# Kernel tuning notes

Measured on AMD Instinct MI355X. Metric: run time of the kernel, lower is better.

The kernel has to match this reference:

```python
import jax, jax.numpy as jnp
import numpy as np

B, HW, ENC = 64, 14, 2048
T_CAP, VOCAB = 25, 10000
EMB = DEC = ATT = 512


def setup_inputs() -> dict:
    key = jax.random.key(0)
    ks = jax.random.split(key, 24)
    n = lambda k, shape, s=0.02: jax.random.normal(k, shape, jnp.float32) * s
    encoder_out = jax.random.normal(ks[0], (B, HW, HW, ENC), jnp.float32)
    captions = jax.random.randint(ks[1], (B, T_CAP), 0, VOCAB)
    lens = jax.random.randint(ks[2], (B,), 2, T_CAP + 1)
    caption_lengths = jnp.sort(lens)[::-1].at[0].set(T_CAP)  # sorted desc, max=T_CAP
    return {
        'encoder_out': encoder_out,
        'captions': captions,
        'caption_lengths': caption_lengths,
        'emb': jax.random.uniform(ks[3], (VOCAB, EMB), jnp.float32, -0.1, 0.1),
        'We_att': n(ks[4], (ENC, ATT)), 'be_att': jnp.zeros((ATT,), jnp.float32),
        'Wd_att': n(ks[5], (DEC, ATT)), 'bd_att': jnp.zeros((ATT,), jnp.float32),
        'v_att': n(ks[6], (ATT, 1)),    'bv_att': jnp.zeros((1,), jnp.float32),
        'W_ih': n(ks[7], (4 * DEC, EMB + ENC)), 'b_ih': jnp.zeros((4 * DEC,), jnp.float32),
        'W_hh': n(ks[8], (4 * DEC, DEC)),       'b_hh': jnp.zeros((4 * DEC,), jnp.float32),
        'W_init_h': n(ks[9], (ENC, DEC)),  'b_init_h': jnp.zeros((DEC,), jnp.float32),
        'W_init_c': n(ks[10], (ENC, DEC)), 'b_init_c': jnp.zeros((DEC,), jnp.float32),
        'W_fbeta': n(ks[11], (DEC, ENC)),  'b_fbeta': jnp.zeros((ENC,), jnp.float32),
        'W_fc': jax.random.uniform(ks[12], (DEC, VOCAB), jnp.float32, -0.1, 0.1),
        'b_fc': jnp.zeros((VOCAB,), jnp.float32),
    }


def reference(encoder_out, captions, caption_lengths, emb,
              We_att, be_att, Wd_att, bd_att, v_att, bv_att,
              W_ih, b_ih, W_hh, b_hh,
              W_init_h, b_init_h, W_init_c, b_init_c,
              W_fbeta, b_fbeta, W_fc, b_fc):
    Bn = encoder_out.shape[0]
    enc = encoder_out.reshape(Bn, -1, encoder_out.shape[-1])  # [B, P=196, ENC]
    decode_lengths = caption_lengths - 1
    T = captions.shape[1] - 1  # static max(decode_lengths)

    emb_cap = emb[captions]                    # [B, T+1, EMB]
    mean_enc = enc.mean(axis=1)                # [B, ENC]
    h0 = mean_enc @ W_init_h + b_init_h        # [B, DEC]
    c0 = mean_enc @ W_init_c + b_init_c
    att1 = enc @ We_att + be_att               # [B, P, ATT], hoisted (same math each step)

    def step(carry, inp):
        h, c = carry
        x_emb, active = inp                    # [B,EMB], [B] bool (batch_size_t mask)
        # attention
        att2 = h @ Wd_att + bd_att             # [B, ATT]
        e = (jax.nn.relu(att1 + att2[:, None, :]) @ v_att)[..., 0] + bv_att[0]  # [B, P]
        alpha = jax.nn.softmax(e, axis=1)
        ctx = jnp.einsum('bp,bpe->be', alpha, enc)
        # gated context
        ctx = jax.nn.sigmoid(h @ W_fbeta + b_fbeta) * ctx
        # LSTMCell (torch gate order i, f, g, o)
        x = jnp.concatenate([x_emb, ctx], axis=1)
        g = x @ W_ih.T + b_ih + h @ W_hh.T + b_hh
        i_g, f_g, g_g, o_g = jnp.split(g, 4, axis=1)
        c_new = jax.nn.sigmoid(f_g) * c + jax.nn.sigmoid(i_g) * jnp.tanh(g_g)
        h_new = jax.nn.sigmoid(o_g) * jnp.tanh(c_new)
        pred = h_new @ W_fc + b_fc             # dropout = identity (eval)
        m = active[:, None]
        pred = jnp.where(m, pred, 0.0)         # padded rows stay zero (as in torch)
        alpha = jnp.where(m, alpha, 0.0)
        h = jnp.where(m, h_new, h)
        c = jnp.where(m, c_new, c)
        return (h, c), (pred, alpha)

    active_ts = jnp.arange(T)[:, None] < decode_lengths[None, :]   # [T, B]
    xs = (jnp.swapaxes(emb_cap[:, :T], 0, 1), active_ts)
    _, (preds, alphas) = jax.lax.scan(step, (h0, c0), xs)
    predictions = jnp.swapaxes(preds, 0, 1)    # [B, T, VOCAB]
    alphas = jnp.swapaxes(alphas, 0, 1)        # [B, T, P]
    return predictions, captions, decode_lengths, alphas
```

## Files before the change

### kernel.cpp

```cpp
#include <hip/hip_runtime.h>
#include <hip/hip_bf16.h>

#define BATCH 64
#define NPIX 196
#define ENCD 2048
#define ATTD 512
#define DECD 512
#define EMBD 512
#define NVOCAB 10000
#define TSTEPS 24
#define KX 3072
#define NPAD 10112

typedef short bf16x8 __attribute__((ext_vector_type(8)));
typedef float f32x4 __attribute__((ext_vector_type(4)));

__device__ inline ushort f2bf(float f) {
    union { float f; unsigned u; } v; v.f = f;
    unsigned r = (v.u + 0x7fff + ((v.u >> 16) & 1)) >> 16;
    return (ushort)r;
}
__device__ inline float bf2f(ushort u) {
    union { unsigned u; float f; } v; v.u = ((unsigned)u) << 16;
    return v.f;
}

__global__ __launch_bounds__(256) void k_prep(
        const float* __restrict__ Wih, const float* __restrict__ Whh,
        const float* __restrict__ Wd, const float* __restrict__ Wfb,
        const float* __restrict__ Wfc, const float* __restrict__ We,
        const float* __restrict__ emb, const int* __restrict__ caps,
        const int* __restrict__ lens,
        ushort* __restrict__ WTj, ushort* __restrict__ BpreT,
        ushort* __restrict__ WfcT, ushort* __restrict__ WeT,
        ushort* __restrict__ embpartb, float* __restrict__ hcacc,
        float* __restrict__ cap_out, float* __restrict__ len_out) {
    __shared__ float tile[64][65];
    int blk = blockIdx.x, tid = threadIdx.x;
    int tx = tid & 63, ty = tid >> 6;
    int fx = tid & 15, fy = tid >> 4;
    if (blk < 2048) {
        int j = blk;
        for (int k = 512 + tid; k < KX; k += 256) {
            float v = (k < 2560) ? Wih[(size_t)j * 2560 + k] : Whh[(size_t)j * 512 + (k - 2560)];
            WTj[(size_t)j * KX + k] = f2bf(v);
        }
        if (blk == 0) {
            for (int i = tid; i < 1664; i += 256) {
                if (i < 1600) cap_out[i] = (float)caps[i];
                else          len_out[i - 1600] = (float)(lens[i - 1600] - 1);
            }
        }
    } else if (blk < 2368) {
        int i = blk - 2048;
        int nb = (i % 40) * 64, kb = (i / 40) * 64;
        for (int s = 0; s < 4; ++s) {
            int k = kb + fy + s * 16;
            int n = nb + fx * 4;
            float4 v = (n < ATTD) ? *(const float4*)(Wd + (size_t)k * ATTD + n)
                                  : *(const float4*)(Wfb + (size_t)k * ENCD + (n - ATTD));
            tile[fy + s * 16][fx * 4 + 0] = v.x;
            tile[fy + s * 16][fx * 4 + 1] = v.y;
            tile[fy + s * 16][fx * 4 + 2] = v.z;
            tile[fy + s * 16][fx * 4 + 3] = v.w;
        }
        __syncthreads();
        for (int s = 0; s < 64; s += 4)
            BpreT[(size_t)(nb + ty + s) * 512 + kb + tx] = f2bf(tile[tx][ty + s]);
    } else if (blk < 3632) {
        int i = blk - 2368;
        int nb = (i % 158) * 64, kb = (i / 158) * 64;
        for (int s = 0; s < 4; ++s) {
            int k = kb + fy + s * 16;
            int n = nb + fx * 4;
            float4 v = make_float4(0.f, 0.f, 0.f, 0.f);
            if (n < NVOCAB) v = *(const float4*)(Wfc + (size_t)k * NVOCAB + n);
            tile[fy + s * 16][fx * 4 + 0] = v.x;
            tile[fy + s * 16][fx * 4 + 1] = v.y;
            tile[fy + s * 16][fx * 4 + 2] = v.z;
            tile[fy + s * 16][fx * 4 + 3] = v.w;
        }
        __syncthreads();
        for (int s = 0; s < 64; s += 4)
            WfcT[(size_t)(nb + ty + s) * 512 + kb + tx] = f2bf(tile[tx][ty + s]);
    } else if (blk < 3888) {
        int i = blk - 3632;
        int nb = (i % 8) * 64, kb = (i / 8) * 64;
        for (int s = 0; s < 4; ++s) {
            int k = kb + fy + s * 16;
            int n = nb + fx * 4;
            float4 v = *(const float4*)(We + (size_t)k * ATTD + n);
            tile[fy + s * 16][fx * 4 + 0] = v.x;
            tile[fy + s * 16][fx * 4 + 1] = v.y;
            tile[fy + s * 16][fx * 4 + 2] = v.z;
            tile[fy + s * 16][fx * 4 + 3] = v.w;
        }
        __syncthreads();
        for (int s = 0; s < 64; s += 4)
            WeT[(size_t)(nb + ty + s) * ENCD + kb + tx] = f2bf(tile[tx][ty + s]);
    } else if (blk < 4656) {
        int i = blk - 3888;
        int r0 = (i % 24) * 64;
        int n0 = (i / 24) * 64;
        int w = tid >> 6, l = tid & 63;
        int m = l & 15, kg = l >> 4;
        int n = n0 + w * 16 + m;
        const float* Bp = Wih + (size_t)n * 2560 + kg * 8;
        int tok[4];
#pragma unroll
        for (int mf = 0; mf < 4; ++mf) {
            int row = r0 + m + mf * 16;
            tok[mf] = caps[(row & 63) * 25 + (row >> 6)];
        }
        f32x4 acc[4] = {};
        for (int k0 = 0; k0 < 512; k0 += 32) {
            float4 b0 = *(const float4*)(Bp + k0);
            float4 b1 = *(const float4*)(Bp + k0 + 4);
            bf16x8 bb;
            bb[0] = f2bf(b0.x); bb[1] = f2bf(b0.y); bb[2] = f2bf(b0.z); bb[3] = f2bf(b0.w);
            bb[4] = f2bf(b1.x); bb[5] = f2bf(b1.y); bb[6] = f2bf(b1.z); bb[7] = f2bf(b1.w);
#pragma unroll
            for (int mf = 0; mf < 4; ++mf) {
                const float* ap = emb + (size_t)tok[mf] * 512 + kg * 8 + k0;
                float4 f0 = *(const float4*)ap;
                float4 f1 = *(const float4*)(ap + 4);
                bf16x8 a;
                a[0] = f2bf(f0.x); a[1] = f2bf(f0.y); a[2] = f2bf(f0.z); a[3] = f2bf(f0.w);
                a[4] = f2bf(f1.x); a[5] = f2bf(f1.y); a[6] = f2bf(f1.z); a[7] = f2bf(f1.w);
                acc[mf] = __builtin_amdgcn_mfma_f32_16x16x32_bf16(a, bb, acc[mf], 0, 0, 0);
            }
        }
#pragma unroll
        for (int mf = 0; mf < 4; ++mf)
#pragma unroll
            for (int r = 0; r < 4; ++r)
                embpartb[(size_t)(r0 + mf * 16 + kg * 4 + r) * 2048 + n] = f2bf(acc[mf][r]);
    } else {
        int i = blk - 4656;
        for (int j = tid; j < 2048; j += 256) hcacc[(size_t)i * 2048 + j] = 0.f;
    }
}

__global__ void k_encconv(const float* __restrict__ enc, ushort* __restrict__ encb) {
    size_t i = ((size_t)blockIdx.x * 256 + threadIdx.x) * 8;
    float4 f0 = *(const float4*)(enc + i);
    float4 f1 = *(const float4*)(enc + i + 4);
    union { bf16x8 v; ushort u[8]; } o;
    o.u[0] = f2bf(f0.x); o.u[1] = f2bf(f0.y); o.u[2] = f2bf(f0.z); o.u[3] = f2bf(f0.w);
    o.u[4] = f2bf(f1.x); o.u[5] = f2bf(f1.y); o.u[6] = f2bf(f1.z); o.u[7] = f2bf(f1.w);
    *(bf16x8*)(encb + i) = o.v;
}

__global__ __launch_bounds__(256) void k_meanb(const ushort* __restrict__ encb,
                                               ushort* __restrict__ meanb) {
    int b = blockIdx.x, half = blockIdx.y;
    int e0 = half * 1024 + threadIdx.x * 4;
    const ushort* ep = encb + (size_t)b * NPIX * ENCD + e0;
    float s0 = 0.f, s1 = 0.f, s2 = 0.f, s3 = 0.f;
#pragma unroll 4
    for (int p = 0; p < NPIX; ++p) {
        ushort4 v = *(const ushort4*)(ep + (size_t)p * ENCD);
        s0 += bf2f(v.x); s1 += bf2f(v.y); s2 += bf2f(v.z); s3 += bf2f(v.w);
    }
    const float sc = 1.0f / NPIX;
    ushort4 o;
    o.x = f2bf(s0 * sc); o.y = f2bf(s1 * sc); o.z = f2bf(s2 * sc); o.w = f2bf(s3 * sc);
    *(ushort4*)(meanb + (size_t)b * ENCD + e0) = o;
}

__global__ __launch_bounds__(256) void k_initp(
        const ushort* __restrict__ meanb,
        const float* __restrict__ Wh, const float* __restrict__ Wc,
        float* __restrict__ hcacc) {
    __shared__ float mm[4][256];
    int bg = blockIdx.x * 4;
    int jy = blockIdx.y;
    int kz = blockIdx.z;
    int tid = threadIdx.x;
    for (int i = tid; i < 1024; i += 256) {
        int qq = i >> 8, k = i & 255;
        mm[qq][k] = bf2f(meanb[(size_t)(bg + qq) * ENCD + kz * 256 + k]);
    }
    __syncthreads();
    int j = jy * 256 + tid;
    const float* W; int col;
    if (j < 512) { W = Wh; col = j; } else { W = Wc; col = j - 512; }
    W += (size_t)(kz * 256) * 512 + col;
    float acc[4] = {};
    for (int k = 0; k < 256; ++k) {
        float w = W[(size_t)k * 512];
#pragma unroll
        for (int qq = 0; qq < 4; ++qq) acc[qq] += mm[qq][k] * w;
    }
#pragma unroll
    for (int qq = 0; qq < 4; ++qq)
        atomicAdd(hcacc + (size_t)(bg + qq) * 1024 + j, acc[qq]);
}

__global__ __launch_bounds__(256) void k_initfin(
        const float* __restrict__ hcacc, const float* __restrict__ bh,
        const float* __restrict__ bc, ushort* __restrict__ hbf,
        float* __restrict__ c) {
    int base = blockIdx.x * 2048;
    for (int i = threadIdx.x; i < 2048; i += 256) {
        int idx = base + i;
        int b = idx >> 10, n = idx & 1023;
        float v = hcacc[idx];
        if (n < 512) hbf[(size_t)b * 512 + n] = f2bf(v + bh[n]);
        else         c[(size_t)b * 512 + (n - 512)] = v + bc[n - 512];
    }
}

__global__ __launch_bounds__(512) void k_att1(
        const ushort* __restrict__ encb, const ushort* __restrict__ WeT,
        const float* __restrict__ be, ushort* __restrict__ att1b) {
    __shared__ float red[4][64][65];
    int bid = blockIdx.x;
    int L = (bid & 7) * 49 + (bid >> 3);
    int mt = L >> 2, nt = L & 3;
    int tid = threadIdx.x;
    int w = tid >> 6, l = tid & 63;
    int q = w & 3, kh = w >> 2;
    int wr = q >> 1, wc = q & 1;
    int m0 = mt * 128 + wr * 64;
    int n0 = nt * 128 + wc * 64;
    int ml = l & 15, kg = l >> 4;
    const ushort* aBase = encb + (size_t)(m0 + ml) * ENCD + kh * 1024 + kg * 8;
    const ushort* bBase = WeT + (size_t)(n0 + ml) * ENCD + kh * 1024 + kg * 8;
    f32x4 acc[4][4] = {};
    for (int k0 = 0; k0 < 1024; k0 += 32) {
        bf16x8 bfr[4], afr[4];
#pragma unroll
        for (int nf = 0; nf < 4; ++nf)
            bfr[nf] = *(const bf16x8*)(bBase + (size_t)nf * 16 * ENCD + k0);
#pragma unroll
        for (int mf = 0; mf < 4; ++mf)
            afr[mf] = *(const bf16x8*)(aBase + (size_t)mf * 16 * ENCD + k0);
#pragma unroll
        for (int mf = 0; mf < 4; ++mf)
#pragma unroll
            for (int nf = 0; nf < 4; ++nf)
                acc[mf][nf] = __builtin_amdgcn_mfma_f32_16x16x32_bf16(afr[mf], bfr[nf], acc[mf][nf], 0, 0, 0);
    }
    if (kh == 1) {
#pragma unroll
        for (int mf = 0; mf < 4; ++mf)
#pragma unroll
            for (int nf = 0; nf < 4; ++nf)
#pragma unroll
                for (int r = 0; r < 4; ++r)
                    red[q][mf * 16 + kg * 4 + r][nf * 16 + ml] = acc[mf][nf][r];
    }
    __syncthreads();
    if (kh == 0) {
#pragma unroll
        for (int mf = 0; mf < 4; ++mf)
#pragma unroll
            for (int nf = 0; nf < 4; ++nf) {
                int col = n0 + nf * 16 + ml;
                float bias = be[col];
#pragma unroll
                for (int r = 0; r < 4; ++r) {
                    int row = m0 + mf * 16 + kg * 4 + r;
                    float v = acc[mf][nf][r] + red[q][mf * 16 + kg * 4 + r][nf * 16 + ml];
                    att1b[(size_t)row * ATTD + col] = f2bf(v + bias);
                }
            }
    }
}

__global__ __launch_bounds__(512) void k_hsmall2(
        const ushort* __restrict__ hb_cur, const ushort* __restrict__ BpreT,
        const float* __restrict__ bd, const float* __restrict__ bfb,
        float* __restrict__ att2, ushort* __restrict__ gateb) {
    __shared__ float part[2][64][68];
    int blk = blockIdx.x;
    int tid = threadIdx.x;
    int w = tid >> 6, l = tid & 63;
    int wq = w & 3, kh = w >> 2;
    int m = l & 15, kg = l >> 4;
    int n = blk * 64 + wq * 16 + m;
    const ushort* B = BpreT + (size_t)n * 512 + kh * 256 + kg * 8;
    const ushort* A = hb_cur + (size_t)m * 512 + kh * 256 + kg * 8;
    f32x4 acc[4] = {};
#pragma unroll
    for (int k0 = 0; k0 < 256; k0 += 32) {
        bf16x8 bfr = *(const bf16x8*)(B + k0);
#pragma unroll
        for (int mf = 0; mf < 4; ++mf) {
            bf16x8 afr = *(const bf16x8*)(A + mf * 16 * 512 + k0);
            acc[mf] = __builtin_amdgcn_mfma_f32_16x16x32_bf16(afr, bfr, acc[mf], 0, 0, 0);
        }
    }
#pragma unroll
    for (int mf = 0; mf < 4; ++mf)
#pragma unroll
        for (int r = 0; r < 4; ++r)
            part[kh][mf * 16 + kg * 4 + r][wq * 16 + m] = acc[mf][r];
    __syncthreads();
    for (int idx = tid; idx < 4096; idx += 512) {
        int b = idx >> 6, nn = idx & 63;
        float v = part[0][b][nn] + part[1][b][nn];
        int ng = blk * 64 + nn;
        if (ng < 512) att2[(size_t)b * 512 + ng] = v + bd[ng];
        else {
            int e = ng - 512;
            gateb[(size_t)b * 2048 + e] = f2bf(1.f / (1.f + __expf(-(v + bfb[e]))));
        }
    }
}

__global__ __launch_bounds__(512) void k_scorectx(
        const ushort* __restrict__ att1b, const float* __restrict__ att2,
        const float* __restrict__ vatt, const float* __restrict__ bv,
        const ushort* __restrict__ gateb, const int* __restrict__ lens,
        const ushort* __restrict__ encb,
        ushort* __restrict__ ctxb, float* __restrict__ alpha_out, int t) {
    __shared__ float ev[200];
    __shared__ float cpart[4][512];
    __shared__ float inv_s;
    int bid = blockIdx.x;
    int b = ((bid & 7) << 3) | ((bid >> 3) & 7);
    int q = bid >> 6;
    int tid = threadIdx.x;
    int w = tid >> 6, l = tid & 63;
    if (t >= lens[b] - 1) {
        if (q == 0 && tid < NPIX)
            alpha_out[((size_t)b * TSTEPS + t) * NPIX + tid] = 0.f;
        return;
    }
    {
        float a2r[8], vvr[8];
        const float* att2b = att2 + (size_t)b * ATTD;
#pragma unroll
        for (int i = 0; i < 8; ++i) {
            a2r[i] = att2b[l * 8 + i];
            vvr[i] = vatt[l * 8 + i];
        }
        float bv0 = bv[0];
        for (int pp = w; pp < NPIX; pp += 8) {
            bf16x8 f = *(const bf16x8*)(att1b + ((size_t)b * NPIX + pp) * ATTD + l * 8);
            float s = 0.f;
#pragma unroll
            for (int i = 0; i < 8; ++i)
                s += fmaxf(bf2f((ushort)f[i]) + a2r[i], 0.f) * vvr[i];
            for (int off = 32; off > 0; off >>= 1) s += __shfl_down(s, off);
            if (l == 0) ev[pp] = s + bv0;
        }
    }
    __syncthreads();
    if (w == 0) {
        float mx = -1e30f;
        for (int pp = l; pp < NPIX; pp += 64) mx = fmaxf(mx, ev[pp]);
        for (int off = 32; off > 0; off >>= 1) mx = fmaxf(mx, __shfl_down(mx, off));
        mx = __shfl(mx, 0);
        float s = 0.f;
        for (int pp = l; pp < NPIX; pp += 64) {
            float e_ = __expf(ev[pp] - mx);
            ev[pp] = e_;
            s += e_;
        }
        for (int off = 32; off > 0; off >>= 1) s += __shfl_down(s, off);
        if (l == 0) inv_s = 1.0f / s;
    }
    __syncthreads();
    float inv = inv_s;
    if (q == 0 && tid < NPIX)
        alpha_out[((size_t)b * TSTEPS + t) * NPIX + tid] = ev[tid] * inv;
    {
        int pg = tid >> 7, th = tid & 127;
        const ushort* ep = encb + (size_t)b * NPIX * ENCD + q * 512 + th * 4;
        float s0 = 0.f, s1 = 0.f, s2 = 0.f, s3 = 0.f;
        for (int pp = pg; pp < NPIX; pp += 4) {
            ushort4 v = *(const ushort4*)(ep + (size_t)pp * ENCD);
            float al = ev[pp];
            s0 += al * bf2f(v.x); s1 += al * bf2f(v.y);
            s2 += al * bf2f(v.z); s3 += al * bf2f(v.w);
        }
        cpart[pg][th * 4 + 0] = s0;
        cpart[pg][th * 4 + 1] = s1;
        cpart[pg][th * 4 + 2] = s2;
        cpart[pg][th * 4 + 3] = s3;
    }
    __syncthreads();
    if (tid < 128) {
        ushort4 g4 = *(const ushort4*)(gateb + (size_t)b * 2048 + q * 512 + tid * 4);
        ushort4 o;
        o.x = f2bf((cpart[0][tid * 4 + 0] + cpart[1][tid * 4 + 0] + cpart[2][tid * 4 + 0] + cpart[3][tid * 4 + 0]) * inv * bf2f(g4.x));
        o.y = f2bf((cpart[0][tid * 4 + 1] + cpart[1][tid * 4 + 1] + cpart[2][tid * 4 + 1] + cpart[3][tid * 4 + 1]) * inv * bf2f(g4.y));
        o.z = f2bf((cpart[0][tid * 4 + 2] + cpart[1][tid * 4 + 2] + cpart[2][tid * 4 + 2] + cpart[3][tid * 4 + 2]) * inv * bf2f(g4.z));
        o.w = f2bf((cpart[0][tid * 4 + 3] + cpart[1][tid * 4 + 3] + cpart[2][tid * 4 + 3] + cpart[3][tid * 4 + 3]) * inv * bf2f(g4.w));
        *(ushort4*)(ctxb + (size_t)b * 2048 + q * 512 + tid * 4) = o;
    }
}

__global__ __launch_bounds__(512) void k_gates2(
        const ushort* __restrict__ ctxb, const ushort* __restrict__ hb_cur,
        const ushort* __restrict__ WTj, const ushort* __restrict__ embpartb,
        const float* __restrict__ bih, const float* __restrict__ bhh,
        const int* __restrict__ lens, float* __restrict__ c,
        ushort* __restrict__ hb_nxt, ushort* __restrict__ hAll, int t) {
    __shared__ float part[8][64][16];
    int g = blockIdx.x;
    int tid = threadIdx.x;
    int w = tid >> 6, l = tid & 63;
    int m = l & 15, kg = l >> 4;
    int jrow = (m >> 2) * 512 + g * 4 + (m & 3);
    const ushort* Brow = WTj + (size_t)jrow * KX;
    f32x4 acc[4] = {};
    {
        const ushort* B = Brow + 512 + w * 256 + kg * 8;
        const ushort* A = ctxb + (size_t)m * 2048 + w * 256 + kg * 8;
#pragma unroll
        for (int k0 = 0; k0 < 256; k0 += 32) {
            bf16x8 bfr = *(const bf16x8*)(B + k0);
#pragma unroll
            for (int mf = 0; mf < 4; ++mf) {
                bf16x8 afr = *(const bf16x8*)(A + (size_t)mf * 16 * 2048 + k0);
                acc[mf] = __builtin_amdgcn_mfma_f32_16x16x32_bf16(afr, bfr, acc[mf], 0, 0, 0);
            }
        }
    }
    {
        const ushort* B = Brow + 2560 + w * 64 + kg * 8;
        const ushort* A = hb_cur + (size_t)m * 512 + w * 64 + kg * 8;
#pragma unroll
        for (int k0 = 0; k0 < 64; k0 += 32) {
            bf16x8 bfr = *(const bf16x8*)(B + k0);
#pragma unroll
            for (int mf = 0; mf < 4; ++mf) {
                bf16x8 afr = *(const bf16x8*)(A + (size_t)mf * 16 * 512 + k0);
                acc[mf] = __builtin_amdgcn_mfma_f32_16x16x32_bf16(afr, bfr, acc[mf], 0, 0, 0);
            }
        }
    }
#pragma unroll
    for (int mf = 0; mf < 4; ++mf)
#pragma unroll
        for (int r = 0; r < 4; ++r)
            part[w][mf * 16 + kg * 4 + r][m] = acc[mf][r];
    __syncthreads();
    if (tid < 256) {
        int bb = tid >> 2, j = tid & 3;
        int d = g * 4 + j;
        float gi = 0.f, gf = 0.f, gg = 0.f, go = 0.f;
#pragma unroll
        for (int w8 = 0; w8 < 8; ++w8) {
            gi += part[w8][bb][j];
            gf += part[w8][bb][4 + j];
            gg += part[w8][bb][8 + j];
            go += part[w8][bb][12 + j];
        }
        ushort hout = hb_cur[(size_t)bb * 512 + d];
        if (t < lens[bb] - 1) {
            const ushort* eb = embpartb + ((size_t)t * 64 + bb) * 2048;
            gi += bf2f(eb[d])        + bih[d]        + bhh[d];
            gf += bf2f(eb[512 + d])  + bih[512 + d]  + bhh[512 + d];
            gg += bf2f(eb[1024 + d]) + bih[1024 + d] + bhh[1024 + d];
            go += bf2f(eb[1536 + d]) + bih[1536 + d] + bhh[1536 + d];
            float cc = c[(size_t)bb * 512 + d];
            float si = 1.f / (1.f + __expf(-gi));
            float sf = 1.f / (1.f + __expf(-gf));
            float so = 1.f / (1.f + __expf(-go));
            float cn = sf * cc + si * tanhf(gg);
            float hn = so * tanhf(cn);
            c[(size_t)bb * 512 + d] = cn;
            hout = f2bf(hn);
        }
        hb_nxt[(size_t)bb * 512 + d] = hout;
        hAll[((size_t)t * 64 + bb) * 512 + d] = hout;
    }
}

__global__ __launch_bounds__(256) void k_predall(
        const ushort* __restrict__ hAll, const ushort* __restrict__ WfcT,
        const float* __restrict__ bfc, const int* __restrict__ lens,
        float* __restrict__ pred) {
    int w = threadIdx.x >> 6, l = threadIdx.x & 63;
    int wr = w >> 1, wc = w & 1;
    int m0 = blockIdx.x * 128 + wr * 64;
    int n0 = blockIdx.y * 128 + wc * 64;
    int ml = l & 15, kg = l >> 4;
    const ushort* aBase = hAll + (size_t)(m0 + ml) * 512 + kg * 8;
    const ushort* bBase = WfcT + (size_t)(n0 + ml) * 512 + kg * 8;
    f32x4 acc[4][4] = {};
#pragma unroll 2
    for (int k0 = 0; k0 < 512; k0 += 32) {
        bf16x8 bfr[4], afr[4];
#pragma unroll
        for (int nf = 0; nf < 4; ++nf)
            bfr[nf] = *(const bf16x8*)(bBase + (size_t)nf * 16 * 512 + k0);
#pragma unroll
        for (int mf = 0; mf < 4; ++mf)
            afr[mf] = *(const bf16x8*)(aBase + (size_t)mf * 16 * 512 + k0);
#pragma unroll
        for (int mf = 0; mf < 4; ++mf)
#pragma unroll
            for (int nf = 0; nf < 4; ++nf)
                acc[mf][nf] = __builtin_amdgcn_mfma_f32_16x16x32_bf16(afr[mf], bfr[nf], acc[mf][nf], 0, 0, 0);
    }
#pragma unroll
    for (int mf = 0; mf < 4; ++mf)
#pragma unroll
        for (int nf = 0; nf < 4; ++nf) {
            int col = n0 + nf * 16 + ml;
            if (col < NVOCAB) {
                float bias = bfc[col];
#pragma unroll
                for (int r = 0; r < 4; ++r) {
                    int row = m0 + mf * 16 + kg * 4 + r;
                    int t = row >> 6, b = row & 63;
                    bool act = t < (lens[b] - 1);
                    pred[((size_t)b * TSTEPS + t) * NVOCAB + col] = act ? acc[mf][nf][r] + bias : 0.f;
                }
            }
        }
}

extern "C" void kernel_launch(void* const* d_in, const int* in_sizes, int n_in,
                              void* d_out, int out_size, void* d_ws, size_t ws_size,
                              hipStream_t stream) {
    const float* enc  = (const float*)d_in[0];
    const int*   caps = (const int*)d_in[1];
    const int*   lens = (const int*)d_in[2];
    const float* emb  = (const float*)d_in[3];
    const float* We   = (const float*)d_in[4];
    const float* be   = (const float*)d_in[5];
    const float* Wd   = (const float*)d_in[6];
    const float* bd   = (const float*)d_in[7];
    const float* vatt = (const float*)d_in[8];
    const float* bv   = (const float*)d_in[9];
    const float* Wih  = (const float*)d_in[10];
    const float* bih  = (const float*)d_in[11];
    const float* Whh  = (const float*)d_in[12];
    const float* bhh  = (const float*)d_in[13];
    const float* Winh = (const float*)d_in[14];
    const float* binh = (const float*)d_in[15];
    const float* Winc = (const float*)d_in[16];
    const float* binc = (const float*)d_in[17];
    const float* Wfb  = (const float*)d_in[18];
    const float* bfb  = (const float*)d_in[19];
    const float* Wfc  = (const float*)d_in[20];
    const float* bfc  = (const float*)d_in[21];

    float* out       = (float*)d_out;
    float* pred_out  = out;
    float* cap_out   = out + 15360000;
    float* len_out   = out + 15361600;
    float* alpha_out = out + 15361664;

    char* p = (char*)d_ws;
    ushort* att1b    = (ushort*)p; p += (size_t)12544 * 512 * 2;
    ushort* WTj      = (ushort*)p; p += (size_t)2048 * KX * 2;
    ushort* WfcT     = (ushort*)p; p += (size_t)NPAD * 512 * 2;
    ushort* BpreT    = (ushort*)p; p += (size_t)2560 * 512 * 2;
    ushort* WeT      = (ushort*)p; p += (size_t)512 * 2048 * 2;
    ushort* embpartb = (ushort*)p; p += (size_t)1536 * 2048 * 2;
    ushort* hAll     = (ushort*)p; p += (size_t)1536 * 512 * 2;
    ushort* ctxb     = (ushort*)p; p += (size_t)64 * 2048 * 2;
    ushort* hb0      = (ushort*)p; p += (size_t)64 * 512 * 2;
    ushort* hb1      = (ushort*)p; p += (size_t)64 * 512 * 2;
    float* c         = (float*)p;  p += (size_t)64 * 512 * 4;
    ushort* meanb    = (ushort*)p; p += (size_t)64 * 2048 * 2;
    float* att2      = (float*)p;  p += (size_t)64 * 512 * 4;
    ushort* gateb    = (ushort*)p; p += (size_t)64 * 2048 * 2;
    ushort* encb     = (ushort*)p; p += (size_t)64 * NPIX * ENCD * 2;
    float* hcacc     = (float*)ctxb;

    k_prep<<<4688, 256, 0, stream>>>(Wih, Whh, Wd, Wfb, Wfc, We, emb, caps, lens,
                                     WTj, BpreT, WfcT, WeT, embpartb, hcacc,
                                     cap_out, len_out);
    k_encconv<<<12544, 256, 0, stream>>>(enc, encb);
    k_meanb<<<dim3(64, 2), 256, 0, stream>>>(encb, meanb);
    k_initp<<<dim3(16, 4, 8), 256, 0, stream>>>(meanb, Winh, Winc, hcacc);
    k_initfin<<<32, 256, 0, stream>>>(hcacc, binh, binc, hb0, c);
    k_att1<<<392, 512, 0, stream>>>(encb, WeT, be, att1b);

    for (int t = 0; t < TSTEPS; ++t) {
        const ushort* hcur = (t & 1) ? hb1 : hb0;
        ushort* hnxt = (t & 1) ? hb0 : hb1;
        k_hsmall2<<<40, 512, 0, stream>>>(hcur, BpreT, bd, bfb, att2, gateb);
        k_scorectx<<<256, 512, 0, stream>>>(att1b, att2, vatt, bv, gateb, lens,
                                            encb, ctxb, alpha_out, t);
        k_gates2<<<128, 512, 0, stream>>>(ctxb, hcur, WTj, embpartb, bih, bhh,
                                          lens, c, hnxt, hAll, t);
    }
    k_predall<<<dim3(12, 79), 256, 0, stream>>>(hAll, WfcT, bfc, lens, pred_out);
}
```

Baseline: 1.778 ms.

## Fuse per-step attention and LSTM kernels into one launch with flag-based inter-block sync

```diff
diff --git a/kernel.cpp b/kernel.cpp
--- a/kernel.cpp
+++ b/kernel.cpp
@@ -34,6 +34,7 @@
         ushort* __restrict__ WTj, ushort* __restrict__ BpreT,
         ushort* __restrict__ WfcT, ushort* __restrict__ WeT,
         ushort* __restrict__ embpartb, float* __restrict__ hcacc,
+        int* __restrict__ flags,
         float* __restrict__ cap_out, float* __restrict__ len_out) {
     __shared__ float tile[64][65];
     int blk = blockIdx.x, tid = threadIdx.x;
@@ -138,6 +139,7 @@
     } else {
         int i = blk - 4656;
         for (int j = tid; j < 2048; j += 256) hcacc[(size_t)i * 2048 + j] = 0.f;
+        if (i == 0 && tid < 64) flags[tid] = 0;
     }
 }
 
@@ -211,24 +213,21 @@
     }
 }
 
-__global__ __launch_bounds__(512) void k_att1(
+__global__ __launch_bounds__(256) void k_att1(
         const ushort* __restrict__ encb, const ushort* __restrict__ WeT,
         const float* __restrict__ be, ushort* __restrict__ att1b) {
-    __shared__ float red[4][64][65];
     int bid = blockIdx.x;
     int L = (bid & 7) * 49 + (bid >> 3);
     int mt = L >> 2, nt = L & 3;
-    int tid = threadIdx.x;
-    int w = tid >> 6, l = tid & 63;
-    int q = w & 3, kh = w >> 2;
-    int wr = q >> 1, wc = q & 1;
+    int w = threadIdx.x >> 6, l = threadIdx.x & 63;
+    int wr = w >> 1, wc = w & 1;
     int m0 = mt * 128 + wr * 64;
     int n0 = nt * 128 + wc * 64;
     int ml = l & 15, kg = l >> 4;
-    const ushort* aBase = encb + (size_t)(m0 + ml) * ENCD + kh * 1024 + kg * 8;
-    const ushort* bBase = WeT + (size_t)(n0 + ml) * ENCD + kh * 1024 + kg * 8;
+    const ushort* aBase = encb + (size_t)(m0 + ml) * ENCD + kg * 8;
+    const ushort* bBase = WeT + (size_t)(n0 + ml) * ENCD + kg * 8;
     f32x4 acc[4][4] = {};
-    for (int k0 = 0; k0 < 1024; k0 += 32) {
+    for (int k0 = 0; k0 < ENCD; k0 += 32) {
         bf16x8 bfr[4], afr[4];
 #pragma unroll
         for (int nf = 0; nf < 4; ++nf)
@@ -242,233 +241,242 @@
             for (int nf = 0; nf < 4; ++nf)
                 acc[mf][nf] = __builtin_amdgcn_mfma_f32_16x16x32_bf16(afr[mf], bfr[nf], acc[mf][nf], 0, 0, 0);
     }
-    if (kh == 1) {
-#pragma unroll
-        for (int mf = 0; mf < 4; ++mf)
-#pragma unroll
-            for (int nf = 0; nf < 4; ++nf)
-#pragma unroll
-                for (int r = 0; r < 4; ++r)
-                    red[q][mf * 16 + kg * 4 + r][nf * 16 + ml] = acc[mf][nf][r];
-    }
-    __syncthreads();
-    if (kh == 0) {
-#pragma unroll
-        for (int mf = 0; mf < 4; ++mf)
-#pragma unroll
-            for (int nf = 0; nf < 4; ++nf) {
-                int col = n0 + nf * 16 + ml;
-                float bias = be[col];
-#pragma unroll
-                for (int r = 0; r < 4; ++r) {
-                    int row = m0 + mf * 16 + kg * 4 + r;
-                    float v = acc[mf][nf][r] + red[q][mf * 16 + kg * 4 + r][nf * 16 + ml];
-                    att1b[(size_t)row * ATTD + col] = f2bf(v + bias);
-                }
-            }
-    }
-}
-
-__global__ __launch_bounds__(512) void k_hsmall2(
-        const ushort* __restrict__ hb_cur, const ushort* __restrict__ BpreT,
+#pragma unroll
+    for (int mf = 0; mf < 4; ++mf)
+#pragma unroll
+        for (int nf = 0; nf < 4; ++nf) {
+            int col = n0 + nf * 16 + ml;
+            float bias = be[col];
+#pragma unroll
+            for (int r = 0; r < 4; ++r) {
+                int row = m0 + mf * 16 + kg * 4 + r;
+                att1b[(size_t)row * ATTD + col] = f2bf(acc[mf][nf][r] + bias);
+            }
+        }
+}
+
+__global__ __launch_bounds__(512) void k_step(
+        const ushort* __restrict__ att1b, const ushort* __restrict__ encb,
+        const ushort* __restrict__ BpreT, const ushort* __restrict__ WTj,
+        const ushort* __restrict__ embpartb,
+        const float* __restrict__ vatt, const float* __restrict__ bv,
         const float* __restrict__ bd, const float* __restrict__ bfb,
-        float* __restrict__ att2, ushort* __restrict__ gateb) {
-    __shared__ float part[2][64][68];
-    int blk = blockIdx.x;
-    int tid = threadIdx.x;
-    int w = tid >> 6, l = tid & 63;
-    int wq = w & 3, kh = w >> 2;
-    int m = l & 15, kg = l >> 4;
-    int n = blk * 64 + wq * 16 + m;
-    const ushort* B = BpreT + (size_t)n * 512 + kh * 256 + kg * 8;
-    const ushort* A = hb_cur + (size_t)m * 512 + kh * 256 + kg * 8;
-    f32x4 acc[4] = {};
-#pragma unroll
-    for (int k0 = 0; k0 < 256; k0 += 32) {
-        bf16x8 bfr = *(const bf16x8*)(B + k0);
-#pragma unroll
-        for (int mf = 0; mf < 4; ++mf) {
-            bf16x8 afr = *(const bf16x8*)(A + mf * 16 * 512 + k0);
-            acc[mf] = __builtin_amdgcn_mfma_f32_16x16x32_bf16(afr, bfr, acc[mf], 0, 0, 0);
-        }
-    }
-#pragma unroll
-    for (int mf = 0; mf < 4; ++mf)
-#pragma unroll
-        for (int r = 0; r < 4; ++r)
-            part[kh][mf * 16 + kg * 4 + r][wq * 16 + m] = acc[mf][r];
-    __syncthreads();
-    for (int idx = tid; idx < 4096; idx += 512) {
-        int b = idx >> 6, nn = idx & 63;
-        float v = part[0][b][nn] + part[1][b][nn];
-        int ng = blk * 64 + nn;
-        if (ng < 512) att2[(size_t)b * 512 + ng] = v + bd[ng];
-        else {
-            int e = ng - 512;
-            gateb[(size_t)b * 2048 + e] = f2bf(1.f / (1.f + __expf(-(v + bfb[e]))));
-        }
-    }
-}
-
-__global__ __launch_bounds__(512) void k_scorectx(
-        const ushort* __restrict__ att1b, const float* __restrict__ att2,
-        const float* __restrict__ vatt, const float* __restrict__ bv,
-        const ushort* __restrict__ gateb, const int* __restrict__ lens,
-        const ushort* __restrict__ encb,
-        ushort* __restrict__ ctxb, float* __restrict__ alpha_out, int t) {
-    __shared__ float ev[200];
-    __shared__ float cpart[4][512];
-    __shared__ float inv_s;
+        const float* __restrict__ bih, const float* __restrict__ bhh,
+        const int* __restrict__ lens,
+        const ushort* __restrict__ hb_cur, ushort* __restrict__ hb_nxt,
+        float* __restrict__ c, ushort* __restrict__ hAll,
+        float* __restrict__ att2, ushort* __restrict__ gateb,
+        ushort* __restrict__ ctxb, float* __restrict__ alpha_out,
+        int* __restrict__ flags, int t) {
+    __shared__ char smem_raw[34816];
     int bid = blockIdx.x;
-    int b = ((bid & 7) << 3) | ((bid >> 3) & 7);
-    int q = bid >> 6;
-    int tid = threadIdx.x;
-    int w = tid >> 6, l = tid & 63;
-    if (t >= lens[b] - 1) {
-        if (q == 0 && tid < NPIX)
-            alpha_out[((size_t)b * TSTEPS + t) * NPIX + tid] = 0.f;
-        return;
-    }
-    {
-        float a2r[8], vvr[8];
-        const float* att2b = att2 + (size_t)b * ATTD;
-#pragma unroll
-        for (int i = 0; i < 8; ++i) {
-            a2r[i] = att2b[l * 8 + i];
-            vvr[i] = vatt[l * 8 + i];
-        }
-        float bv0 = bv[0];
-        for (int pp = w; pp < NPIX; pp += 8) {
-            bf16x8 f = *(const bf16x8*)(att1b + ((size_t)b * NPIX + pp) * ATTD + l * 8);
-            float s = 0.f;
-#pragma unroll
-            for (int i = 0; i < 8; ++i)
-                s += fmaxf(bf2f((ushort)f[i]) + a2r[i], 0.f) * vvr[i];
-            for (int off = 32; off > 0; off >>= 1) s += __shfl_down(s, off);
-            if (l == 0) ev[pp] = s + bv0;
-        }
-    }
-    __syncthreads();
-    if (w == 0) {
-        float mx = -1e30f;
-        for (int pp = l; pp < NPIX; pp += 64) mx = fmaxf(mx, ev[pp]);
-        for (int off = 32; off > 0; off >>= 1) mx = fmaxf(mx, __shfl_down(mx, off));
-        mx = __shfl(mx, 0);
-        float s = 0.f;
-        for (int pp = l; pp < NPIX; pp += 64) {
-            float e_ = __expf(ev[pp] - mx);
-            ev[pp] = e_;
-            s += e_;
-        }
-        for (int off = 32; off > 0; off >>= 1) s += __shfl_down(s, off);
-        if (l == 0) inv_s = 1.0f / s;
-    }
-    __syncthreads();
-    float inv = inv_s;
-    if (q == 0 && tid < NPIX)
-        alpha_out[((size_t)b * TSTEPS + t) * NPIX + tid] = ev[tid] * inv;
-    {
-        int pg = tid >> 7, th = tid & 127;
-        const ushort* ep = encb + (size_t)b * NPIX * ENCD + q * 512 + th * 4;
-        float s0 = 0.f, s1 = 0.f, s2 = 0.f, s3 = 0.f;
-        for (int pp = pg; pp < NPIX; pp += 4) {
-            ushort4 v = *(const ushort4*)(ep + (size_t)pp * ENCD);
-            float al = ev[pp];
-            s0 += al * bf2f(v.x); s1 += al * bf2f(v.y);
-            s2 += al * bf2f(v.z); s3 += al * bf2f(v.w);
-        }
-        cpart[pg][th * 4 + 0] = s0;
-        cpart[pg][th * 4 + 1] = s1;
-        cpart[pg][th * 4 + 2] = s2;
-        cpart[pg][th * 4 + 3] = s3;
-    }
-    __syncthreads();
-    if (tid < 128) {
-        ushort4 g4 = *(const ushort4*)(gateb + (size_t)b * 2048 + q * 512 + tid * 4);
-        ushort4 o;
-        o.x = f2bf((cpart[0][tid * 4 + 0] + cpart[1][tid * 4 + 0] + cpart[2][tid * 4 + 0] + cpart[3][tid * 4 + 0]) * inv * bf2f(g4.x));
-        o.y = f2bf((cpart[0][tid * 4 + 1] + cpart[1][tid * 4 + 1] + cpart[2][tid * 4 + 1] + cpart[3][tid * 4 + 1]) * inv * bf2f(g4.y));
-        o.z = f2bf((cpart[0][tid * 4 + 2] + cpart[1][tid * 4 + 2] + cpart[2][tid * 4 + 2] + cpart[3][tid * 4 + 2]) * inv * bf2f(g4.z));
-        o.w = f2bf((cpart[0][tid * 4 + 3] + cpart[1][tid * 4 + 3] + cpart[2][tid * 4 + 3] + cpart[3][tid * 4 + 3]) * inv * bf2f(g4.w));
-        *(ushort4*)(ctxb + (size_t)b * 2048 + q * 512 + tid * 4) = o;
-    }
-}
-
-__global__ __launch_bounds__(512) void k_gates2(
-        const ushort* __restrict__ ctxb, const ushort* __restrict__ hb_cur,
-        const ushort* __restrict__ WTj, const ushort* __restrict__ embpartb,
-        const float* __restrict__ bih, const float* __restrict__ bhh,
-        const int* __restrict__ lens, float* __restrict__ c,
-        ushort* __restrict__ hb_nxt, ushort* __restrict__ hAll, int t) {
-    __shared__ float part[8][64][16];
-    int g = blockIdx.x;
     int tid = threadIdx.x;
     int w = tid >> 6, l = tid & 63;
     int m = l & 15, kg = l >> 4;
-    int jrow = (m >> 2) * 512 + g * 4 + (m & 3);
-    const ushort* Brow = WTj + (size_t)jrow * KX;
-    f32x4 acc[4] = {};
-    {
-        const ushort* B = Brow + 512 + w * 256 + kg * 8;
-        const ushort* A = ctxb + (size_t)m * 2048 + w * 256 + kg * 8;
+    int* flag0 = flags + 2 * t;
+    int* flag1 = flags + 2 * t + 1;
+
+    if (bid < 40) {
+        float (*part)[64][68] = (float (*)[64][68])smem_raw;
+        int blk = bid;
+        int wq = w & 3, kh = w >> 2;
+        int n = blk * 64 + wq * 16 + m;
+        const ushort* B = BpreT + (size_t)n * 512 + kh * 256 + kg * 8;
+        const ushort* A = hb_cur + (size_t)m * 512 + kh * 256 + kg * 8;
+        f32x4 acc[4] = {};
 #pragma unroll
         for (int k0 = 0; k0 < 256; k0 += 32) {
             bf16x8 bfr = *(const bf16x8*)(B + k0);
 #pragma unroll
             for (int mf = 0; mf < 4; ++mf) {
-                bf16x8 afr = *(const bf16x8*)(A + (size_t)mf * 16 * 2048 + k0);
+                bf16x8 afr = *(const bf16x8*)(A + mf * 16 * 512 + k0);
                 acc[mf] = __builtin_amdgcn_mfma_f32_16x16x32_bf16(afr, bfr, acc[mf], 0, 0, 0);
             }
         }
-    }
-    {
-        const ushort* B = Brow + 2560 + w * 64 + kg * 8;
-        const ushort* A = hb_cur + (size_t)m * 512 + w * 64 + kg * 8;
-#pragma unroll
-        for (int k0 = 0; k0 < 64; k0 += 32) {
-            bf16x8 bfr = *(const bf16x8*)(B + k0);
-#pragma unroll
-            for (int mf = 0; mf < 4; ++mf) {
-                bf16x8 afr = *(const bf16x8*)(A + (size_t)mf * 16 * 512 + k0);
-                acc[mf] = __builtin_amdgcn_mfma_f32_16x16x32_bf16(afr, bfr, acc[mf], 0, 0, 0);
-            }
-        }
-    }
-#pragma unroll
-    for (int mf = 0; mf < 4; ++mf)
-#pragma unroll
-        for (int r = 0; r < 4; ++r)
-            part[w][mf * 16 + kg * 4 + r][m] = acc[mf][r];
-    __syncthreads();
-    if (tid < 256) {
-        int bb = tid >> 2, j = tid & 3;
-        int d = g * 4 + j;
-        float gi = 0.f, gf = 0.f, gg = 0.f, go = 0.f;
-#pragma unroll
-        for (int w8 = 0; w8 < 8; ++w8) {
-            gi += part[w8][bb][j];
-            gf += part[w8][bb][4 + j];
-            gg += part[w8][bb][8 + j];
-            go += part[w8][bb][12 + j];
-        }
-        ushort hout = hb_cur[(size_t)bb * 512 + d];
-        if (t < lens[bb] - 1) {
-            const ushort* eb = embpartb + ((size_t)t * 64 + bb) * 2048;
-            gi += bf2f(eb[d])        + bih[d]        + bhh[d];
-            gf += bf2f(eb[512 + d])  + bih[512 + d]  + bhh[512 + d];
-            gg += bf2f(eb[1024 + d]) + bih[1024 + d] + bhh[1024 + d];
-            go += bf2f(eb[1536 + d]) + bih[1536 + d] + bhh[1536 + d];
-            float cc = c[(size_t)bb * 512 + d];
-            float si = 1.f / (1.f + __expf(-gi));
-            float sf = 1.f / (1.f + __expf(-gf));
-            float so = 1.f / (1.f + __expf(-go));
-            float cn = sf * cc + si * tanhf(gg);
-            float hn = so * tanhf(cn);
-            c[(size_t)bb * 512 + d] = cn;
-            hout = f2bf(hn);
-        }
-        hb_nxt[(size_t)bb * 512 + d] = hout;
-        hAll[((size_t)t * 64 + bb) * 512 + d] = hout;
+#pragma unroll
+        for (int mf = 0; mf < 4; ++mf)
+#pragma unroll
+            for (int r = 0; r < 4; ++r)
+                part[kh][mf * 16 + kg * 4 + r][wq * 16 + m] = acc[mf][r];
+        __syncthreads();
+        for (int idx = tid; idx < 4096; idx += 512) {
+            int b = idx >> 6, nn = idx & 63;
+            float v = part[0][b][nn] + part[1][b][nn];
+            int ng = blk * 64 + nn;
+            if (ng < 512) att2[(size_t)b * 512 + ng] = v + bd[ng];
+            else {
+                int e = ng - 512;
+                gateb[(size_t)b * 2048 + e] = f2bf(1.f / (1.f + __expf(-(v + bfb[e]))));
+            }
+        }
+        __syncthreads();
+        if (tid == 0) {
+            __threadfence();
+            __hip_atomic_fetch_add(flag0, 1, __ATOMIC_RELEASE, __HIP_MEMORY_SCOPE_AGENT);
+        }
+    } else if (bid < 296) {
+        float* ev = (float*)smem_raw;
+        float* cpart = ev + 200;
+        float* inv_sp = cpart + 2048;
+        int bid2 = bid - 40;
+        int b = ((bid2 & 7) << 3) | ((bid2 >> 3) & 7);
+        int q = bid2 >> 6;
+        if (t >= lens[b] - 1) {
+            if (q == 0 && tid < NPIX)
+                alpha_out[((size_t)b * TSTEPS + t) * NPIX + tid] = 0.f;
+            __syncthreads();
+            if (tid == 0) {
+                __threadfence();
+                __hip_atomic_fetch_add(flag1, 1, __ATOMIC_RELEASE, __HIP_MEMORY_SCOPE_AGENT);
+            }
+            return;
+        }
+        float vvr[8];
+#pragma unroll
+        for (int i = 0; i < 8; ++i) vvr[i] = vatt[l * 8 + i];
+        float bv0 = bv[0];
+        if (tid == 0) {
+            while (__hip_atomic_load(flag0, __ATOMIC_ACQUIRE, __HIP_MEMORY_SCOPE_AGENT) < 40)
+                __builtin_amdgcn_s_sleep(8);
+        }
+        __syncthreads();
+        {
+            float a2r[8];
+            const float* att2b = att2 + (size_t)b * ATTD;
+#pragma unroll
+            for (int i = 0; i < 8; ++i) a2r[i] = att2b[l * 8 + i];
+            for (int pp = w; pp < NPIX; pp += 8) {
+                bf16x8 f = *(const bf16x8*)(att1b + ((size_t)b * NPIX + pp) * ATTD + l * 8);
+                float s = 0.f;
+#pragma unroll
+                for (int i = 0; i < 8; ++i)
+                    s += fmaxf(bf2f((ushort)f[i]) + a2r[i], 0.f) * vvr[i];
+                for (int off = 32; off > 0; off >>= 1) s += __shfl_down(s, off);
+                if (l == 0) ev[pp] = s + bv0;
+            }
+        }
+        __syncthreads();
+        if (w == 0) {
+            float mx = -1e30f;
+            for (int pp = l; pp < NPIX; pp += 64) mx = fmaxf(mx, ev[pp]);
+            for (int off = 32; off > 0; off >>= 1) mx = fmaxf(mx, __shfl_down(mx, off));
+            mx = __shfl(mx, 0);
+            float s = 0.f;
+            for (int pp = l; pp < NPIX; pp += 64) {
+                float e_ = __expf(ev[pp] - mx);
+                ev[pp] = e_;
+                s += e_;
+            }
+            for (int off = 32; off > 0; off >>= 1) s += __shfl_down(s, off);
+            if (l == 0) *inv_sp = 1.0f / s;
+        }
+        __syncthreads();
+        float inv = *inv_sp;
+        if (q == 0 && tid < NPIX)
+            alpha_out[((size_t)b * TSTEPS + t) * NPIX + tid] = ev[tid] * inv;
+        {
+            int pg = tid >> 7, th = tid & 127;
+            const ushort* ep = encb + (size_t)b * NPIX * ENCD + q * 512 + th * 4;
+            float s0 = 0.f, s1 = 0.f, s2 = 0.f, s3 = 0.f;
+            for (int pp = pg; pp < NPIX; pp += 4) {
+                ushort4 v = *(const ushort4*)(ep + (size_t)pp * ENCD);
+                float al = ev[pp];
+                s0 += al * bf2f(v.x); s1 += al * bf2f(v.y);
+                s2 += al * bf2f(v.z); s3 += al * bf2f(v.w);
+            }
+            cpart[pg * 512 + th * 4 + 0] = s0;
+            cpart[pg * 512 + th * 4 + 1] = s1;
+            cpart[pg * 512 + th * 4 + 2] = s2;
+            cpart[pg * 512 + th * 4 + 3] = s3;
+        }
+        __syncthreads();
+        if (tid < 128) {
+            ushort4 g4 = *(const ushort4*)(gateb + (size_t)b * 2048 + q * 512 + tid * 4);
+            ushort4 o;
+            o.x = f2bf((cpart[tid * 4 + 0] + cpart[512 + tid * 4 + 0] + cpart[1024 + tid * 4 + 0] + cpart[1536 + tid * 4 + 0]) * inv * bf2f(g4.x));
+            o.y = f2bf((cpart[tid * 4 + 1] + cpart[512 + tid * 4 + 1] + cpart[1024 + tid * 4 + 1] + cpart[1536 + tid * 4 + 1]) * inv * bf2f(g4.y));
+            o.z = f2bf((cpart[tid * 4 + 2] + cpart[512 + tid * 4 + 2] + cpart[1024 + tid * 4 + 2] + cpart[1536 + tid * 4 + 2]) * inv * bf2f(g4.z));
+            o.w = f2bf((cpart[tid * 4 + 3] + cpart[512 + tid * 4 + 3] + cpart[1024 + tid * 4 + 3] + cpart[1536 + tid * 4 + 3]) * inv * bf2f(g4.w));
+            *(ushort4*)(ctxb + (size_t)b * 2048 + q * 512 + tid * 4) = o;
+        }
+        __syncthreads();
+        if (tid == 0) {
+            __threadfence();
+            __hip_atomic_fetch_add(flag1, 1, __ATOMIC_RELEASE, __HIP_MEMORY_SCOPE_AGENT);
+        }
+    } else {
+        float (*part)[64][16] = (float (*)[64][16])smem_raw;
+        int g = bid - 296;
+        int jrow = (m >> 2) * 512 + g * 4 + (m & 3);
+        const ushort* Brow = WTj + (size_t)jrow * KX;
+        if (tid == 0) {
+            while (__hip_atomic_load(flag1, __ATOMIC_ACQUIRE, __HIP_MEMORY_SCOPE_AGENT) < 256)
+                __builtin_amdgcn_s_sleep(8);
+        }
+        __syncthreads();
+        f32x4 acc[4] = {};
+        {
+            const ushort* B = Brow + 512 + w * 256 + kg * 8;
+            const ushort* A = ctxb + (size_t)m * 2048 + w * 256 + kg * 8;
+#pragma unroll
+            for (int k0 = 0; k0 < 256; k0 += 32) {
+                bf16x8 bfr = *(const bf16x8*)(B + k0);
+#pragma unroll
+                for (int mf = 0; mf < 4; ++mf) {
+                    bf16x8 afr = *(const bf16x8*)(A + (size_t)mf * 16 * 2048 + k0);
+                    acc[mf] = __builtin_amdgcn_mfma_f32_16x16x32_bf16(afr, bfr, acc[mf], 0, 0, 0);
+                }
+            }
+        }
+        {
+            const ushort* B = Brow + 2560 + w * 64 + kg * 8;
+            const ushort* A = hb_cur + (size_t)m * 512 + w * 64 + kg * 8;
+#pragma unroll
+            for (int k0 = 0; k0 < 64; k0 += 32) {
+                bf16x8 bfr = *(const bf16x8*)(B + k0);
+#pragma unroll
+                for (int mf = 0; mf < 4; ++mf) {
+                    bf16x8 afr = *(const bf16x8*)(A + (size_t)mf * 16 * 512 + k0);
+                    acc[mf] = __builtin_amdgcn_mfma_f32_16x16x32_bf16(afr, bfr, acc[mf], 0, 0, 0);
+                }
+            }
+        }
+#pragma unroll
+        for (int mf = 0; mf < 4; ++mf)
+#pragma unroll
+            for (int r = 0; r < 4; ++r)
+                part[w][mf * 16 + kg * 4 + r][m] = acc[mf][r];
+        __syncthreads();
+        if (tid < 256) {
+            int bb = tid >> 2, j = tid & 3;
+            int d = g * 4 + j;
+            float gi = 0.f, gf = 0.f, gg = 0.f, go = 0.f;
+#pragma unroll
+            for (int w8 = 0; w8 < 8; ++w8) {
+                gi += part[w8][bb][j];
+                gf += part[w8][bb][4 + j];
+                gg += part[w8][bb][8 + j];
+                go += part[w8][bb][12 + j];
+            }
+            ushort hout = hb_cur[(size_t)bb * 512 + d];
+            if (t < lens[bb] - 1) {
+                const ushort* eb = embpartb + ((size_t)t * 64 + bb) * 2048;
+                gi += bf2f(eb[d])        + bih[d]        + bhh[d];
+                gf += bf2f(eb[512 + d])  + bih[512 + d]  + bhh[512 + d];
+                gg += bf2f(eb[1024 + d]) + bih[1024 + d] + bhh[1024 + d];
+                go += bf2f(eb[1536 + d]) + bih[1536 + d] + bhh[1536 + d];
+                float cc = c[(size_t)bb * 512 + d];
+                float si = 1.f / (1.f + __expf(-gi));
+                float sf = 1.f / (1.f + __expf(-gf));
+                float so = 1.f / (1.f + __expf(-go));
+                float cn = sf * cc + si * tanhf(gg);
+                float hn = so * tanhf(cn);
+                c[(size_t)bb * 512 + d] = cn;
+                hout = f2bf(hn);
+            }
+            hb_nxt[(size_t)bb * 512 + d] = hout;
+            hAll[((size_t)t * 64 + bb) * 512 + d] = hout;
+        }
     }
 }
 
@@ -564,26 +572,26 @@
     ushort* meanb    = (ushort*)p; p += (size_t)64 * 2048 * 2;
     float* att2      = (float*)p;  p += (size_t)64 * 512 * 4;
     ushort* gateb    = (ushort*)p; p += (size_t)64 * 2048 * 2;
+    int* flags       = (int*)p;    p += (size_t)64 * 4;
     ushort* encb     = (ushort*)p; p += (size_t)64 * NPIX * ENCD * 2;
     float* hcacc     = (float*)ctxb;
 
     k_prep<<<4688, 256, 0, stream>>>(Wih, Whh, Wd, Wfb, Wfc, We, emb, caps, lens,
-                                     WTj, BpreT, WfcT, WeT, embpartb, hcacc,
+                                     WTj, BpreT, WfcT, WeT, embpartb, hcacc, flags,
                                      cap_out, len_out);
     k_encconv<<<12544, 256, 0, stream>>>(enc, encb);
     k_meanb<<<dim3(64, 2), 256, 0, stream>>>(encb, meanb);
     k_initp<<<dim3(16, 4, 8), 256, 0, stream>>>(meanb, Winh, Winc, hcacc);
     k_initfin<<<32, 256, 0, stream>>>(hcacc, binh, binc, hb0, c);
-    k_att1<<<392, 512, 0, stream>>>(encb, WeT, be, att1b);
+    k_att1<<<392, 256, 0, stream>>>(encb, WeT, be, att1b);
 
     for (int t = 0; t < TSTEPS; ++t) {
         const ushort* hcur = (t & 1) ? hb1 : hb0;
         ushort* hnxt = (t & 1) ? hb0 : hb1;
-        k_hsmall2<<<40, 512, 0, stream>>>(hcur, BpreT, bd, bfb, att2, gateb);
-        k_scorectx<<<256, 512, 0, stream>>>(att1b, att2, vatt, bv, gateb, lens,
-                                            encb, ctxb, alpha_out, t);
-        k_gates2<<<128, 512, 0, stream>>>(ctxb, hcur, WTj, embpartb, bih, bhh,
-                                          lens, c, hnxt, hAll, t);
+        k_step<<<424, 512, 0, stream>>>(att1b, encb, BpreT, WTj, embpartb,
+                                        vatt, bv, bd, bfb, bih, bhh, lens,
+                                        hcur, hnxt, c, hAll, att2, gateb, ctxb,
+                                        alpha_out, flags, t);
     }
     k_predall<<<dim3(12, 79), 256, 0, stream>>>(hAll, WfcT, bfc, lens, pred_out);
 }
```

After: 3.991 ms. 124% more time.
